# Optimization experiments

Measured on AMD Instinct MI355X. Metric: run time of the kernel, lower is better.

The kernel has to match this reference:

```python
import jax, jax.numpy as jnp
import numpy as np

B, S, D, U, E = 64, 512, 1024, 4096, 16


def setup_inputs() -> dict:
    key = jax.random.key(0)
    k1, k2, k3 = jax.random.split(key, 3)
    x = jax.random.normal(k1, (B, S, D), dtype=jnp.float32)
    index = jax.random.randint(k2, (B, 1), 0, E, dtype=jnp.int32)
    # glorot_uniform for (E, D, U) kernel
    limit = np.sqrt(6.0 / (D + U)).astype(np.float32)
    ws = jax.random.uniform(k3, (E, D, U), dtype=jnp.float32, minval=-limit, maxval=limit)
    bs = jnp.zeros((E, U), dtype=jnp.float32)
    return {"x": x, "ws": ws, "bs": bs, "index": index}


def reference(x, ws, bs, index):
    # tf.gather_nd(ws, index) with index shape (B, 1) == ws[index[:, 0]]
    idx = index[:, 0]                      # [B]
    w = ws[idx]                            # [B, D, U] per-group expert weights
    b = bs[idx]                            # [B, U]
    # einsum 'adb,abc->adc' in the original == bsd,bdu->bsu here
    out = jnp.einsum('bsd,bdu->bsu', x, w) + b[:, None, :]
    return jax.nn.relu(out)
```

## Files before the change

### kernel.cpp

```cpp
#include <hip/hip_runtime.h>


typedef float v4f  __attribute__((ext_vector_type(4)));
typedef _Float16 v8h __attribute__((ext_vector_type(8)));
typedef __fp16  v2fp __attribute__((ext_vector_type(2)));

constexpr int Bb = 64, Ss = 512, Dd = 1024, Uu = 4096, Ee = 16;

typedef const __attribute__((address_space(1))) void gvoid_t;
typedef __attribute__((address_space(3))) void lvoid_t;
__device__ __forceinline__ void gl2lds16(const void* g, void* l) {
  __builtin_amdgcn_global_load_lds((gvoid_t*)g, (lvoid_t*)l, 16, 0, 0);
}

#define BAR()  asm volatile("s_barrier" ::: "memory")
#define LGK0() asm volatile("s_waitcnt lgkmcnt(0)" ::: "memory")
#define VMW(n) asm volatile("s_waitcnt vmcnt(" #n ")" ::: "memory")

__global__ void perm_kernel(const int* __restrict__ index, int* __restrict__ perm,
                            int* __restrict__ used) {
  const int b = threadIdx.x;
  const int e = index[b];
  int pos = 0;
  for (int b2 = 0; b2 < Bb; ++b2) {
    const int e2 = index[b2];
    pos += (e2 < e) || (e2 == e && b2 < b);
  }
  perm[pos] = b;
  if (used != nullptr && b < Ee) {
    int u = 0;
    for (int b2 = 0; b2 < Bb; ++b2) u |= (index[b2] == b) ? 1 : 0;
    used[b] = u;
  }
}

__global__ __launch_bounds__(256) void convert_x(const float* __restrict__ in,
                                                 _Float16* __restrict__ outh) {
  const size_t i = ((size_t)blockIdx.x * 256 + threadIdx.x) * 8;
  const v4f a = *(const v4f*)(in + i);
  const v4f b = *(const v4f*)(in + i + 4);
  v8h h;
  #pragma unroll
  for (int j = 0; j < 4; ++j) h[j] = (_Float16)a[j];
  #pragma unroll
  for (int j = 0; j < 4; ++j) h[4 + j] = (_Float16)b[j];
  *(v8h*)(outh + i) = h;
}

__global__ __launch_bounds__(256) void transpose_w(const float* __restrict__ ws,
                                                   _Float16* __restrict__ wt,
                                                   const int* __restrict__ used) {
  const int e = blockIdx.z;
  if (!used[e]) return;
  const int u0 = blockIdx.x * 64;
  const int d0 = blockIdx.y * 64;
  __shared__ float tile[64][65];
  const int tid = threadIdx.x;
  {
    const int tu = (tid & 15) * 4;
    const int td = tid >> 4;
    const float* src = ws + (size_t)e * Dd * Uu + (size_t)d0 * Uu + u0;
    #pragma unroll
    for (int i = 0; i < 4; ++i) {
      const v4f v = *(const v4f*)(src + (size_t)(td + i * 16) * Uu + tu);
      tile[td + i * 16][tu + 0] = v[0];
      tile[td + i * 16][tu + 1] = v[1];
      tile[td + i * 16][tu + 2] = v[2];
      tile[td + i * 16][tu + 3] = v[3];
    }
  }
  __syncthreads();
  {
    const int tu = tid >> 2;
    const int tq = (tid & 3) * 16;
    _Float16* dst = wt + (size_t)e * Uu * Dd + (size_t)(u0 + tu) * Dd + d0 + tq;
    v8h h0, h1;
    #pragma unroll
    for (int j = 0; j < 8; ++j) h0[j] = (_Float16)tile[tq + j][tu];
    #pragma unroll
    for (int j = 0; j < 8; ++j) h1[j] = (_Float16)tile[tq + 8 + j][tu];
    *(v8h*)dst = h0;
    *(v8h*)(dst + 8) = h1;
  }
}

__global__ __launch_bounds__(512, 2) void gemm_8p(
    const _Float16* __restrict__ xh, const _Float16* __restrict__ wt,
    const float* __restrict__ bs, const int* __restrict__ index,
    const int* __restrict__ perm, float* __restrict__ out) {
  extern __shared__ _Float16 lds[];
  constexpr int A0 = 0, A1 = 16384, B0 = 32768, B1 = 49152;
  constexpr int NIT = 8;

  const int bx = blockIdx.x;
  const int by = blockIdx.y;
  const int bz = perm[blockIdx.z];
  const int e  = index[bz];

  const int tid  = threadIdx.x;
  const int lane = tid & 63;
  const int wave = tid >> 6;
  const int wr = wave >> 2, wc = wave & 3;
  const int fl = lane & 15, fq = lane >> 4;

  const _Float16* Ag = xh + ((size_t)bz * Ss + by * 256) * Dd;
  const _Float16* Bg = wt + ((size_t)e  * Uu + bx * 256) * Dd;
  const float* bias  = bs + (size_t)e * Uu + bx * 256;
  float* C = out + (size_t)bz * Ss * Uu + (size_t)(by * 256) * Uu + bx * 256;

  auto stageHT = [&](int ldsBase, const _Float16* g, int half) {
    #pragma unroll
    for (int i = 0; i < 2; ++i) {
      const int cb = i * 512 + wave * 64;
      const int c  = cb + lane;
      const int r  = half * 128 + (c >> 3);
      const int sc = (c & 7) ^ (r & 7);
      gl2lds16(g + (size_t)r * Dd + sc * 8, &lds[ldsBase + half * 8192 + cb * 8]);
    }
  };

  const int aswz0 = ((0 + fq) ^ (fl & 7)) * 8;
  const int aswz1 = ((4 + fq) ^ (fl & 7)) * 8;

  v8h ar[4][2];
  v8h br[4][2];
  auto ldA = [&](int base, int mh) {
    const int r0 = wr * 128 + mh * 64 + fl;
    #pragma unroll
    for (int mi = 0; mi < 4; ++mi) {
      ar[mi][0] = *(const v8h*)&lds[base + (r0 + mi * 16) * 64 + aswz0];
      ar[mi][1] = *(const v8h*)&lds[base + (r0 + mi * 16) * 64 + aswz1];
    }
  };
  auto ldB = [&](int base, int nh) {
    const int r0 = wc * 64 + nh * 32 + fl;
    #pragma unroll
    for (int nl = 0; nl < 2; ++nl) {
      br[nh * 2 + nl][0] = *(const v8h*)&lds[base + (r0 + nl * 16) * 64 + aswz0];
      br[nh * 2 + nl][1] = *(const v8h*)&lds[base + (r0 + nl * 16) * 64 + aswz1];
    }
  };

  v4f acc[8][4];
  #pragma unroll
  for (int i = 0; i < 8; ++i)
    #pragma unroll
    for (int j = 0; j < 4; ++j) acc[i][j] = {0.f, 0.f, 0.f, 0.f};

  auto mm = [&](int mh, int nh) {
    __builtin_amdgcn_s_setprio(1);
    #pragma unroll
    for (int mi = 0; mi < 4; ++mi)
      #pragma unroll
      for (int nl = 0; nl < 2; ++nl) {
        const int gi = mh * 4 + mi, ni = nh * 2 + nl;
        acc[gi][ni] = __builtin_amdgcn_mfma_f32_16x16x32_f16(ar[mi][0], br[ni][0], acc[gi][ni], 0, 0, 0);
        acc[gi][ni] = __builtin_amdgcn_mfma_f32_16x16x32_f16(ar[mi][1], br[ni][1], acc[gi][ni], 0, 0, 0);
      }
    __builtin_amdgcn_s_setprio(0);
  };

  stageHT(A0, Ag, 0); stageHT(A0, Ag, 1);
  stageHT(B0, Bg, 0); stageHT(B0, Bg, 1);
  stageHT(A1, Ag + 64, 0);
  VMW(2); BAR();

  for (int t = 0; t < NIT; ++t) {
    const _Float16* Ao  = Ag + (2 * t + 1) * 64;
    const _Float16* Bo  = Bg + (2 * t + 1) * 64;
    const _Float16* Ae2 = Ag + (2 * t + 2) * 64;
    const _Float16* Be2 = Bg + (2 * t + 2) * 64;
    const _Float16* Ao3 = Ag + (2 * t + 3) * 64;
    const bool st = (t < NIT - 1);

    ldA(A0, 0); ldB(B0, 0);
    stageHT(A1, Ao, 1);
    BAR(); LGK0(); mm(0, 0); BAR();
    ldB(B0, 1);
    stageHT(B1, Bo, 0);
    BAR(); LGK0(); mm(0, 1); BAR();
    ldA(A0, 1);
    stageHT(B1, Bo, 1);
    BAR(); LGK0(); mm(1, 0); BAR();
    if (st) stageHT(A0, Ae2, 0);
    BAR(); LGK0(); mm(1, 1);
    if (st) { VMW(2); } else { VMW(0); }
    BAR();

    ldA(A1, 0); ldB(B1, 0);
    if (st) stageHT(A0, Ae2, 1);
    BAR(); LGK0(); mm(0, 0); BAR();
    ldB(B1, 1);
    if (st) stageHT(B0, Be2, 0);
    BAR(); LGK0(); mm(0, 1); BAR();
    ldA(A1, 1);
    if (st) stageHT(B0, Be2, 1);
    BAR(); LGK0(); mm(1, 0); BAR();
    if (st) stageHT(A1, Ao3, 0);
    BAR(); LGK0(); mm(1, 1);
    if (st) { VMW(2); }
    BAR();
  }

  float bv[4];
  #pragma unroll
  for (int ni = 0; ni < 4; ++ni) bv[ni] = bias[wc * 64 + ni * 16 + fl];

  #pragma unroll
  for (int gi = 0; gi < 8; ++gi) {
    #pragma unroll
    for (int r = 0; r < 4; ++r) {
      const int row = wr * 128 + gi * 16 + fq * 4 + r;
      float* crow = C + (size_t)row * Uu + wc * 64 + fl;
      #pragma unroll
      for (int ni = 0; ni < 4; ++ni) {
        const float v = acc[gi][ni][r] + bv[ni];
        crow[ni * 16] = fmaxf(v, 0.0f);
      }
    }
  }
}

__global__ __launch_bounds__(256) void indexed_dense_gemm_h(
    const _Float16* __restrict__ xh, const _Float16* __restrict__ wt,
    const float* __restrict__ bs, const int* __restrict__ index,
    const int* __restrict__ perm, float* __restrict__ out) {
  constexpr int BM = 128, BN = 128, BK = 32, KT = Dd / BK;
  const int bx = blockIdx.x;
  const int by = blockIdx.y;
  const int bz = perm[blockIdx.z];
  const int e  = index[bz];

  const int tid  = threadIdx.x;
  const int lane = tid & 63;
  const int wave = tid >> 6;

  const _Float16* A  = xh + (size_t)bz * (Ss * Dd) + (size_t)(by * BM) * Dd;
  const _Float16* Bt = wt + (size_t)e * (Dd * Uu) + (size_t)(bx * BN) * Dd;
  const float* bias  = bs + (size_t)e * Uu + bx * BN;
  float*       C     = out + (size_t)bz * Ss * Uu + (size_t)(by * BM) * Uu + bx * BN;

  __shared__ __align__(16) _Float16 As [2][BM * BK];
  __shared__ __align__(16) _Float16 Bsh[2][BN * BK];

  const int c0 = wave * 64;
  auto stage = [&](int buf, int kt) {
    const _Float16* a = A  + kt * BK;
    const _Float16* b = Bt + kt * BK;
    #pragma unroll
    for (int i = 0; i < 2; ++i) {
      const int cb  = c0 + i * 256;
      const int cl  = cb + lane;
      const int row = cl >> 2;
      const int kq  = (cl & 3) * 8;
      gl2lds16(a + (size_t)row * Dd + kq, &As [buf][cb * 8]);
      gl2lds16(b + (size_t)row * Dd + kq, &Bsh[buf][cb * 8]);
    }
  };

  const int fl = lane & 15;
  const int fq = lane >> 4;
  const int wm = (wave >> 1) * 64;
  const int wn = (wave & 1) * 64;
  const int aOff = (wm + fl) * BK + fq * 8;
  const int bOff = (wn + fl) * BK + fq * 8;

  v4f acc[4][4];
  #pragma unroll
  for (int i = 0; i < 4; ++i)
    #pragma unroll
    for (int j = 0; j < 4; ++j) acc[i][j] = {0.f, 0.f, 0.f, 0.f};

  stage(0, 0);
  __syncthreads();

  int buf = 0;
  for (int kt = 0; kt < KT; ++kt) {
    if (kt + 1 < KT) stage(buf ^ 1, kt + 1);

    v8h afr[4], bfr[4];
    #pragma unroll
    for (int mt = 0; mt < 4; ++mt) afr[mt] = *(const v8h*)&As [buf][aOff + mt * 16 * BK];
    #pragma unroll
    for (int nt = 0; nt < 4; ++nt) bfr[nt] = *(const v8h*)&Bsh[buf][bOff + nt * 16 * BK];

    #pragma unroll
    for (int mt = 0; mt < 4; ++mt)
      #pragma unroll
      for (int nt = 0; nt < 4; ++nt)
        acc[mt][nt] = __builtin_amdgcn_mfma_f32_16x16x32_f16(afr[mt], bfr[nt], acc[mt][nt], 0, 0, 0);

    if (kt + 1 < KT) {
      __syncthreads();
      buf ^= 1;
    }
  }

  float bv[4];
  #pragma unroll
  for (int nt = 0; nt < 4; ++nt) bv[nt] = bias[wn + nt * 16 + fl];

  const int row0 = wm + fq * 4;
  #pragma unroll
  for (int mt = 0; mt < 4; ++mt) {
    #pragma unroll
    for (int r = 0; r < 4; ++r) {
      float* crow = C + (size_t)(row0 + mt * 16 + r) * Uu + wn + fl;
      #pragma unroll
      for (int nt = 0; nt < 4; ++nt) {
        const float v = acc[mt][nt][r] + bv[nt];
        crow[nt * 16] = fmaxf(v, 0.0f);
      }
    }
  }
}

__global__ __launch_bounds__(256) void indexed_dense_gemm(
    const float* __restrict__ x, const float* __restrict__ ws,
    const float* __restrict__ bs, const int* __restrict__ index,
    const int* __restrict__ perm, float* __restrict__ out) {
  constexpr int BM = 128, BN = 128, BK = 32, KT = Dd / BK, BKP = 40;
  const int bx = blockIdx.x;
  const int by = blockIdx.y;
  const int bz = perm[blockIdx.z];
  const int e  = index[bz];

  const int tid  = threadIdx.x;
  const int lane = tid & 63;
  const int wave = tid >> 6;

  const float* A    = x   + (size_t)bz * (Ss * Dd) + (size_t)(by * BM) * Dd;
  const float* W    = ws  + (size_t)e * (Dd * Uu) + bx * BN;
  const float* bias = bs  + (size_t)e * Uu + bx * BN;
  float*       C    = out + (size_t)bz * Ss * Uu + (size_t)(by * BM) * Uu + bx * BN;

  __shared__ __align__(16) _Float16 As[BM * BKP];
  __shared__ __align__(16) _Float16 Bs[BN * BKP];

  const int am  = tid >> 1;
  const int ak0 = (tid & 1) * 16;
  const float* Aptr = A + am * Dd + ak0;
  _Float16* aWr = &As[am * BKP + ak0];

  const int bn  = (wave & 1) * 64 + lane;
  const int bk0 = (wave >> 1) * 16;
  const float* Wptr = W + (size_t)bk0 * Uu + bn;
  _Float16* bWr = &Bs[bn * BKP + bk0];

  const int fl = lane & 15;
  const int fq = lane >> 4;
  const int wm = (wave >> 1) * 64;
  const int wn = (wave & 1) * 64;
  const _Float16* aRd = &As[(wm + fl) * BKP + fq * 8];
  const _Float16* bRd = &Bs[(wn + fl) * BKP + fq * 8];

  v4f acc[4][4];
  #pragma unroll
  for (int i = 0; i < 4; ++i)
    #pragma unroll
    for (int j = 0; j < 4; ++j) acc[i][j] = {0.f, 0.f, 0.f, 0.f};

  v4f   aReg[4];
  float bReg[16];

  auto loadTile = [&](int kt) {
    const float* p = Aptr + kt * BK;
    #pragma unroll
    for (int i = 0; i < 4; ++i) aReg[i] = ((const v4f*)p)[i];
    const float* q = Wptr + (size_t)kt * (BK * Uu);
    #pragma unroll
    for (int j = 0; j < 16; ++j) bReg[j] = q[(size_t)j * Uu];
  };

  auto stage = [&]() {
    union { v8h v[2]; v2fp h[8]; } ua;
    const float* af = (const float*)aReg;
    #pragma unroll
    for (int i = 0; i < 8; ++i)
      ua.h[i] = __builtin_amdgcn_cvt_pkrtz(af[2 * i], af[2 * i + 1]);
    *(v8h*)(aWr)     = ua.v[0];
    *(v8h*)(aWr + 8) = ua.v[1];

    union { v8h v[2]; v2fp h[8]; } ub;
    #pragma unroll
    for (int i = 0; i < 8; ++i)
      ub.h[i] = __builtin_amdgcn_cvt_pkrtz(bReg[2 * i], bReg[2 * i + 1]);
    *(v8h*)(bWr)     = ub.v[0];
    *(v8h*)(bWr + 8) = ub.v[1];
  };

  loadTile(0);
  stage();
  __syncthreads();

  for (int kt = 0; kt < KT; ++kt) {
    if (kt + 1 < KT) loadTile(kt + 1);

    v8h afr[4], bfr[4];
    #pragma unroll
    for (int mt = 0; mt < 4; ++mt) afr[mt] = *(const v8h*)(aRd + mt * 16 * BKP);
    #pragma unroll
    for (int nt = 0; nt < 4; ++nt) bfr[nt] = *(const v8h*)(bRd + nt * 16 * BKP);

    #pragma unroll
    for (int mt = 0; mt < 4; ++mt)
      #pragma unroll
      for (int nt = 0; nt < 4; ++nt)
        acc[mt][nt] = __builtin_amdgcn_mfma_f32_16x16x32_f16(afr[mt], bfr[nt], acc[mt][nt], 0, 0, 0);

    __syncthreads();
    if (kt + 1 < KT) stage();
    __syncthreads();
  }

  float bv[4];
  #pragma unroll
  for (int nt = 0; nt < 4; ++nt) bv[nt] = bias[wn + nt * 16 + fl];

  const int row0 = wm + fq * 4;
  #pragma unroll
  for (int mt = 0; mt < 4; ++mt) {
    #pragma unroll
    for (int r = 0; r < 4; ++r) {
      float* crow = C + (size_t)(row0 + mt * 16 + r) * Uu + wn + fl;
      #pragma unroll
      for (int nt = 0; nt < 4; ++nt) {
        const float v = acc[mt][nt][r] + bv[nt];
        crow[nt * 16] = fmaxf(v, 0.0f);
      }
    }
  }
}

extern "C" void kernel_launch(void* const* d_in, const int* in_sizes, int n_in,
                              void* d_out, int out_size, void* d_ws, size_t ws_size,
                              hipStream_t stream) {
  const float* x    = (const float*)d_in[0];
  const float* wsP  = (const float*)d_in[1];
  const float* bsP  = (const float*)d_in[2];
  const int*   idx  = (const int*)d_in[3];
  float*       out  = (float*)d_out;

  const size_t szW  = (size_t)Ee * Dd * Uu * sizeof(_Float16);
  const size_t szX  = (size_t)Bb * Ss * Dd * sizeof(_Float16);
  const size_t need = szW + szX + 1024;

  static bool bigLds = [] {
    return hipFuncSetAttribute(reinterpret_cast<const void*>(gemm_8p),
                               hipFuncAttributeMaxDynamicSharedMemorySize,
                               131072) == hipSuccess;
  }();

  if (ws_size >= need) {
    _Float16* wt  = (_Float16*)d_ws;
    _Float16* xh  = (_Float16*)((char*)d_ws + szW);
    int* perm = (int*)((char*)d_ws + szW + szX);
    int* used = perm + Bb;

    perm_kernel<<<1, 64, 0, stream>>>(idx, perm, used);
    convert_x<<<(Bb * Ss * Dd) / (256 * 8), 256, 0, stream>>>(x, xh);
    transpose_w<<<dim3(Uu / 64, Dd / 64, Ee), 256, 0, stream>>>(wsP, wt, used);

    if (bigLds) {
      dim3 grid(Uu / 256, Ss / 256, Bb);
      gemm_8p<<<grid, 512, 131072, stream>>>(xh, wt, bsP, idx, perm, out);
    } else {
      dim3 grid(Uu / 128, Ss / 128, Bb);
      indexed_dense_gemm_h<<<grid, 256, 0, stream>>>(xh, wt, bsP, idx, perm, out);
    }
  } else {
    int* perm = (int*)d_ws;
    perm_kernel<<<1, 64, 0, stream>>>(idx, perm, nullptr);
    dim3 grid(Uu / 128, Ss / 128, Bb);
    indexed_dense_gemm<<<grid, 256, 0, stream>>>(x, wsP, bsP, idx, perm, out);
  }
}
```

Measured before the change: 1.016 ms.

## Restructure GEMM LDS pipeline into two-stage stripe prefetch and nontemporal output stores

```diff
diff --git a/kernel.cpp b/kernel.cpp
--- a/kernel.cpp
+++ b/kernel.cpp
@@ -89,8 +89,8 @@
     const float* __restrict__ bs, const int* __restrict__ index,
     const int* __restrict__ perm, float* __restrict__ out) {
   extern __shared__ _Float16 lds[];
-  constexpr int A0 = 0, A1 = 16384, B0 = 32768, B1 = 49152;
-  constexpr int NIT = 8;
+  constexpr int Abase = 0, Bbase = 32768;
+  constexpr int KT = 16;
 
   const int bx = blockIdx.x;
   const int by = blockIdx.y;
@@ -108,15 +108,11 @@
   const float* bias  = bs + (size_t)e * Uu + bx * 256;
   float* C = out + (size_t)bz * Ss * Uu + (size_t)(by * 256) * Uu + bx * 256;
 
-  auto stageHT = [&](int ldsBase, const _Float16* g, int half) {
-    #pragma unroll
-    for (int i = 0; i < 2; ++i) {
-      const int cb = i * 512 + wave * 64;
-      const int c  = cb + lane;
-      const int r  = half * 128 + (c >> 3);
-      const int sc = (c & 7) ^ (r & 7);
-      gl2lds16(g + (size_t)r * Dd + sc * 8, &lds[ldsBase + half * 8192 + cb * 8]);
-    }
+  auto stageStripe = [&](int ldsHalfBase, const _Float16* gRow0) {
+    const int c = wave * 64 + lane;
+    const int r = c >> 3;
+    const int s = (c & 7) ^ (r & 7);
+    gl2lds16(gRow0 + (size_t)r * Dd + s * 8, &lds[ldsHalfBase + wave * 512]);
   };
 
   const int aswz0 = ((0 + fq) ^ (fl & 7)) * 8;
@@ -160,45 +156,47 @@
     __builtin_amdgcn_s_setprio(0);
   };
 
-  stageHT(A0, Ag, 0); stageHT(A0, Ag, 1);
-  stageHT(B0, Bg, 0); stageHT(B0, Bg, 1);
-  stageHT(A1, Ag + 64, 0);
-  VMW(2); BAR();
-
-  for (int t = 0; t < NIT; ++t) {
-    const _Float16* Ao  = Ag + (2 * t + 1) * 64;
-    const _Float16* Bo  = Bg + (2 * t + 1) * 64;
-    const _Float16* Ae2 = Ag + (2 * t + 2) * 64;
-    const _Float16* Be2 = Bg + (2 * t + 2) * 64;
-    const _Float16* Ao3 = Ag + (2 * t + 3) * 64;
-    const bool st = (t < NIT - 1);
-
-    ldA(A0, 0); ldB(B0, 0);
-    stageHT(A1, Ao, 1);
+  #pragma unroll
+  for (int j = 0; j < 4; ++j) stageStripe(Abase + j * 4096,         Ag + (size_t)(j * 64) * Dd);
+  #pragma unroll
+  for (int j = 0; j < 4; ++j) stageStripe(Bbase + j * 4096,         Bg + (size_t)(j * 64) * Dd);
+  #pragma unroll
+  for (int j = 0; j < 4; ++j) stageStripe(Abase + 16384 + j * 4096, Ag + (size_t)(j * 64) * Dd + 64);
+  #pragma unroll
+  for (int j = 0; j < 4; ++j) stageStripe(Bbase + 16384 + j * 4096, Bg + (size_t)(j * 64) * Dd + 64);
+  VMW(8); BAR();
+
+  for (int kt = 0; kt < KT; ++kt) {
+    const int aB = Abase + (kt & 1) * 16384;
+    const int bB = Bbase + (kt & 1) * 16384;
+    const bool st2 = (kt + 2 < KT);
+    const bool st1 = (kt + 1 < KT);
+    const _Float16* A2 = Ag + (kt + 2) * 64;
+    const _Float16* B2 = Bg + (kt + 2) * 64;
+
+    ldA(aB, 0); ldB(bB, 0);
     BAR(); LGK0(); mm(0, 0); BAR();
-    ldB(B0, 1);
-    stageHT(B1, Bo, 0);
+    ldB(bB, 1);
+    if (st2) {
+      stageStripe(aB + 0 * 4096, A2);
+      stageStripe(aB + 2 * 4096, A2 + (size_t)128 * Dd);
+    }
     BAR(); LGK0(); mm(0, 1); BAR();
-    ldA(A0, 1);
-    stageHT(B1, Bo, 1);
+    ldA(aB, 1);
+    if (st2) {
+      stageStripe(bB + 0 * 4096, B2);
+      stageStripe(bB + 1 * 4096, B2 + (size_t)64 * Dd);
+      stageStripe(bB + 2 * 4096, B2 + (size_t)128 * Dd);
+      stageStripe(bB + 3 * 4096, B2 + (size_t)192 * Dd);
+    }
     BAR(); LGK0(); mm(1, 0); BAR();
-    if (st) stageHT(A0, Ae2, 0);
-    BAR(); LGK0(); mm(1, 1);
-    if (st) { VMW(2); } else { VMW(0); }
-    BAR();
-
-    ldA(A1, 0); ldB(B1, 0);
-    if (st) stageHT(A0, Ae2, 1);
-    BAR(); LGK0(); mm(0, 0); BAR();
-    ldB(B1, 1);
-    if (st) stageHT(B0, Be2, 0);
-    BAR(); LGK0(); mm(0, 1); BAR();
-    ldA(A1, 1);
-    if (st) stageHT(B0, Be2, 1);
-    BAR(); LGK0(); mm(1, 0); BAR();
-    if (st) stageHT(A1, Ao3, 0);
-    BAR(); LGK0(); mm(1, 1);
-    if (st) { VMW(2); }
+    if (st2) {
+      stageStripe(aB + 1 * 4096, A2 + (size_t)64 * Dd);
+      stageStripe(aB + 3 * 4096, A2 + (size_t)192 * Dd);
+    }
+    BAR(); mm(1, 1);
+    if (st2)      { VMW(8); }
+    else if (st1) { VMW(0); }
     BAR();
   }
 
@@ -215,7 +213,7 @@
       #pragma unroll
       for (int ni = 0; ni < 4; ++ni) {
         const float v = acc[gi][ni][r] + bv[ni];
-        crow[ni * 16] = fmaxf(v, 0.0f);
+        __builtin_nontemporal_store(fmaxf(v, 0.0f), crow + ni * 16);
       }
     }
   }
```

New measurement: 1.030 ms. Within noise of the previous version (+1.3%).
